# Performance work log

Hardware: AMD Instinct MI355X
Metric: run time of the kernel (lower is better)

## Reference

```python
import jax, jax.numpy as jnp
import numpy as np

D_MODEL = 1024
NHEAD = 16
HEAD_DIM = D_MODEL // NHEAD
ROPE_BASE = 10000.0


def setup_inputs() -> dict:
    key = jax.random.key(0)
    k1, k2, k3 = jax.random.split(key, 3)
    b, t = 2, 2048
    x = jax.random.normal(k1, (b, t, D_MODEL), dtype=jnp.float32)
    # weights stored as [in, out] so projection is x @ W (math-equivalent to torch Linear)
    w_qkv = jax.random.normal(k2, (D_MODEL, 3 * D_MODEL), dtype=jnp.float32) * (D_MODEL ** -0.5)
    w_out = jax.random.normal(k3, (D_MODEL, D_MODEL), dtype=jnp.float32) * (D_MODEL ** -0.5)
    return {"x": x, "w_qkv": w_qkv, "w_out": w_out}


def _rotate_half(x):
    # interleaved even/odd rotation, faithful to the torch code
    x1 = x[..., ::2]
    x2 = x[..., 1::2]
    return jnp.stack([-x2, x1], axis=-1).reshape(x.shape)


def _rope_cache(seq_len, dtype):
    half = HEAD_DIM // 2
    inv_freq = 1.0 / (ROPE_BASE ** (jnp.arange(half, dtype=jnp.float32) / float(half)))
    t = jnp.arange(seq_len, dtype=jnp.float32)
    freqs = jnp.einsum("i,j->ij", t, inv_freq)          # [T, half]
    emb = jnp.concatenate([freqs, freqs], axis=-1)        # [T, head_dim]
    return jnp.cos(emb).astype(dtype), jnp.sin(emb).astype(dtype)


def reference(x, w_qkv, w_out):
    b, t, c = x.shape
    qkv = x @ w_qkv                                       # [B, T, 3C]
    q, k, v = jnp.split(qkv, 3, axis=-1)
    def heads(z):
        return z.reshape(b, t, NHEAD, HEAD_DIM).transpose(0, 2, 1, 3)  # [B, H, T, Dh]
    q, k, v = heads(q), heads(k), heads(v)
    cos, sin = _rope_cache(t, q.dtype)                    # [T, Dh] broadcast over B, H
    q = q * cos + _rotate_half(q) * sin
    k = k * cos + _rotate_half(k) * sin
    scale = 1.0 / jnp.sqrt(jnp.asarray(HEAD_DIM, dtype=q.dtype))
    scores = jnp.einsum("bhqd,bhkd->bhqk", q, k) * scale  # [B, H, T, T]
    attn = jax.nn.softmax(scores, axis=-1)
    y = jnp.einsum("bhqk,bhkd->bhqd", attn, v)            # [B, H, T, Dh]
    y = y.transpose(0, 2, 1, 3).reshape(b, t, c)
    return y @ w_out
```

## Files before the change

### kernel.cpp

```cpp
#include <hip/hip_runtime.h>

typedef unsigned short u16;
typedef unsigned int u32;
typedef float f32x4 __attribute__((ext_vector_type(4)));
typedef float f32x16 __attribute__((ext_vector_type(16)));
typedef unsigned int u32x2 __attribute__((ext_vector_type(2)));
typedef __bf16 bf16x8 __attribute__((ext_vector_type(8)));

using gas_ptr = const __attribute__((address_space(1))) void*;
using las_ptr = __attribute__((address_space(3))) void*;

#define NH 16
#define HD 64
#define TSEQ 2048

__device__ __forceinline__ u16 f2bf(float f) {
  return __builtin_bit_cast(u16, (__bf16)f);
}
__device__ __forceinline__ u32 pk2bf(float a, float b) {
  return (u32)f2bf(a) | ((u32)f2bf(b) << 16);
}
__device__ __forceinline__ void pl_swap(u32& a, u32& b) {
  auto r = __builtin_amdgcn_permlane32_swap(a, b, false, false);
  u32x2 rv = __builtin_bit_cast(u32x2, r);
  a = rv[0];
  b = rv[1];
}

template <int NI>
__device__ __forceinline__ void stage_rows(const u16* __restrict__ src, size_t rstride,
                                           int row0, int col0, u16* lbuf, int tid) {
#pragma unroll
  for (int i = 0; i < NI; ++i) {
    int p = i * 256 + tid;
    int r = p >> 3, cst = p & 7;
    int csrc = cst ^ (r & 7);
    const u16* g = src + (size_t)(row0 + r) * rstride + col0 + csrc * 8;
    char* l = (char*)lbuf + (size_t)(i * 256 + (tid & ~63)) * 16;
    __builtin_amdgcn_global_load_lds((gas_ptr)g, (las_ptr)l, 16, 0, 0);
  }
}

__global__ void k_f32_to_bf16(const float* __restrict__ in, u16* __restrict__ out, int n4) {
  int i = blockIdx.x * blockDim.x + threadIdx.x;
  if (i >= n4) return;
  float4 v = ((const float4*)in)[i];
  ((uint2*)out)[i] = make_uint2(pk2bf(v.x, v.y), pk2bf(v.z, v.w));
}

__global__ void k_rope_tab(float2* __restrict__ tab) {
  int i = blockIdx.x * 256 + threadIdx.x;
  int t = i >> 5, j = i & 31;
  float inv = exp2f(-(float)j * 0.41524101186092028f);
  float s, c;
  sincosf((float)t * inv, &s, &c);
  tab[i] = make_float2(c, s);
}

__global__ void k_transpose_bf16(const float* __restrict__ in, u16* __restrict__ out,
                                 int R, int C) {
  __shared__ u16 lds[64 * 68];
  const int t = threadIdx.x;
  const int c0 = blockIdx.x * 64, r0 = blockIdx.y * 64;
  const int fc = (t & 15) * 4;
#pragma unroll
  for (int p = 0; p < 4; ++p) {
    int r = p * 16 + (t >> 4);
    float4 v = *(const float4*)&in[(size_t)(r0 + r) * C + c0 + fc];
    *(uint2*)&lds[r * 68 + fc] = make_uint2(pk2bf(v.x, v.y), pk2bf(v.z, v.w));
  }
  __syncthreads();
#pragma unroll
  for (int p = 0; p < 16; ++p) {
    int c = p * 4 + (t >> 6);
    int r = t & 63;
    out[(size_t)(c0 + c) * R + r0 + r] = lds[r * 68 + c];
  }
}

template <int MODE>
__global__ __launch_bounds__(256, 2) void k_gemm(const u16* __restrict__ A,
                                                 const u16* __restrict__ B,
                                                 float* __restrict__ outF,
                                                 u16* __restrict__ qb, u16* __restrict__ kb,
                                                 u16* __restrict__ vb,
                                                 const float2* __restrict__ rt, int N) {
  __shared__ __align__(16) u16 SH[32768];
  u16* Alb = SH;
  u16* Blb = SH + 16384;
  const int tid = threadIdx.x;
  const int lane = tid & 63;
  const int wv = tid >> 6, wr = wv >> 1, wc = wv & 1;
  const int m0 = blockIdx.y * 128, n0 = blockIdx.x * 128;

  f32x4 acc[4][4] = {};

  stage_rows<4>(A, 1024, m0, 0, Alb, tid);
  stage_rows<4>(B, 1024, n0, 0, Blb, tid);
  __syncthreads();

  for (int kt = 0; kt < 16; ++kt) {
    const int cur = kt & 1;
    if (kt < 15) {
      stage_rows<4>(A, 1024, m0, (kt + 1) * 64, Alb + (cur ^ 1) * 8192, tid);
      stage_rows<4>(B, 1024, n0, (kt + 1) * 64, Blb + (cur ^ 1) * 8192, tid);
    }
#pragma unroll
    for (int ks = 0; ks < 2; ++ks) {
      bf16x8 af[4], bfr[4];
#pragma unroll
      for (int mi = 0; mi < 4; ++mi) {
        int r = wr * 64 + mi * 16 + (lane & 15);
        int ch = (ks * 4 + (lane >> 4)) ^ (r & 7);
        af[mi] = *(const bf16x8*)((const char*)(Alb + cur * 8192) + r * 128 + ch * 16);
      }
#pragma unroll
      for (int ni = 0; ni < 4; ++ni) {
        int r = wc * 64 + ni * 16 + (lane & 15);
        int ch = (ks * 4 + (lane >> 4)) ^ (r & 7);
        bfr[ni] = *(const bf16x8*)((const char*)(Blb + cur * 8192) + r * 128 + ch * 16);
      }
#pragma unroll
      for (int mi = 0; mi < 4; ++mi)
#pragma unroll
        for (int ni = 0; ni < 4; ++ni)
          acc[mi][ni] =
              __builtin_amdgcn_mfma_f32_16x16x32_bf16(af[mi], bfr[ni], acc[mi][ni], 0, 0, 0);
    }
    __syncthreads();
  }

  if constexpr (MODE == 0) {
    const int which = n0 >> 10;
    u16* TB = SH;
    if (which < 2) {
      const float c0 = 0.18033688011112043f;
#pragma unroll
      for (int mi = 0; mi < 4; ++mi) {
        const int mb = wr * 64 + mi * 16 + ((lane >> 4) << 2);
#pragma unroll
        for (int ni = 0; ni < 4; ++ni) {
          const int nl = wc * 64 + ni * 16 + (lane & 15);
          const int d = (n0 + nl) & 63;
          const float sgn = (d & 1) ? 1.0f : -1.0f;
#pragma unroll
          for (int rr = 0; rr < 4; ++rr) {
            float v = acc[mi][ni][rr];
            float vp = __shfl_xor(v, 1);
            int tg = (m0 + mb + rr) & 2047;
            float2 cs = rt[tg * 32 + (d & 31)];
            float rv = v * cs.x + sgn * vp * cs.y;
            if (which == 0) rv *= c0;
            TB[(mb + rr) * 136 + nl] = f2bf(rv);
          }
        }
      }
      __syncthreads();
      const int m = tid >> 1, halfc = tid & 1;
      u16* dst = (which == 0 ? qb : kb) + (size_t)(m0 + m) * 1024 + (n0 & 1023) + halfc * 64;
      const u16* src = TB + m * 136 + halfc * 64;
#pragma unroll
      for (int j = 0; j < 8; ++j) *(uint4*)(dst + j * 8) = *(const uint4*)(src + j * 8);
    } else {
#pragma unroll
      for (int mi = 0; mi < 4; ++mi) {
        const int mb = wr * 64 + mi * 16 + ((lane >> 4) << 2);
#pragma unroll
        for (int ni = 0; ni < 4; ++ni) {
          const int nl = wc * 64 + ni * 16 + (lane & 15);
          uint2 w = make_uint2(pk2bf(acc[mi][ni][0], acc[mi][ni][1]),
                               pk2bf(acc[mi][ni][2], acc[mi][ni][3]));
          *(uint2*)(TB + nl * 136 + mb) = w;
        }
      }
      __syncthreads();
      const int nrow = tid >> 1, halfc = tid & 1;
      const int d = nrow & 63;
      const int hI = ((n0 - 2048) >> 6) + (nrow >> 6);
      const int bI = m0 >> 11;
      const int tb0 = (m0 & 2047) + halfc * 64;
      u16* dst = vb + ((size_t)((bI * NH + hI) * HD + d)) * TSEQ + tb0;
      const u16* src = TB + nrow * 136 + halfc * 64;
#pragma unroll
      for (int j = 0; j < 8; ++j) *(uint4*)(dst + j * 8) = *(const uint4*)(src + j * 8);
    }
  } else {
#pragma unroll
    for (int mi = 0; mi < 4; ++mi) {
      const int m = m0 + wr * 64 + mi * 16 + ((lane >> 4) << 2);
#pragma unroll
      for (int ni = 0; ni < 4; ++ni) {
        const int n = n0 + wc * 64 + ni * 16 + (lane & 15);
#pragma unroll
        for (int rr = 0; rr < 4; ++rr) outF[(size_t)(m + rr) * N + n] = acc[mi][ni][rr];
      }
    }
  }
}

__global__ __launch_bounds__(256, 2) void k_attn(const u16* __restrict__ qbuf,
                                                 const u16* __restrict__ kbuf,
                                                 const u16* __restrict__ vbuf,
                                                 u16* __restrict__ ybuf) {
  __shared__ __align__(16) u16 Kl[2][64 * 64];
  __shared__ __align__(16) u16 Vl[2][64 * 64];
  const int tid = threadIdx.x, lane = tid & 63, wv = tid >> 6;
  const int di = blockIdx.x;
  const int bh = (di & 7) * 4 + ((di >> 3) & 3);
  const int qt = di >> 5;
  const int b = bh >> 4, h = bh & 15;
  const int l31 = lane & 31, hi = lane >> 5;

  const u16* qrow = qbuf + (size_t)(b * TSEQ + qt * 128 + wv * 32 + l31) * 1024 + h * HD;
  const u16* kbase = kbuf + (size_t)b * TSEQ * 1024 + h * HD;
  const u16* vbase = vbuf + (size_t)bh * HD * TSEQ;

  bf16x8 qf[4];
#pragma unroll
  for (int s = 0; s < 4; ++s) qf[s] = *(const bf16x8*)(qrow + s * 16 + hi * 8);

  f32x16 o[2] = {};
  float psum = 0.f;

  stage_rows<2>(kbase, 1024, 0, 0, Kl[0], tid);
  stage_rows<2>(vbase, TSEQ, 0, 0, Vl[0], tid);
  __syncthreads();

  for (int it = 0; it < 32; ++it) {
    const int cur = it & 1;
    if (it < 31) {
      stage_rows<2>(kbase, 1024, (it + 1) * 64, 0, Kl[cur ^ 1], tid);
      stage_rows<2>(vbase, TSEQ, 0, (it + 1) * 64, Vl[cur ^ 1], tid);
    }
    bf16x8 pa[4];
#pragma unroll
    for (int kvt = 0; kvt < 2; ++kvt) {
      f32x16 sa = {};
#pragma unroll
      for (int s = 0; s < 4; ++s) {
        int r = kvt * 32 + l31;
        int ch = (s * 2 + hi) ^ (r & 7);
        bf16x8 kf = *(const bf16x8*)((const char*)Kl[cur] + r * 128 + ch * 16);
        sa = __builtin_amdgcn_mfma_f32_32x32x16_bf16(kf, qf[s], sa, 0, 0, 0);
      }
      float p[16];
#pragma unroll
      for (int r = 0; r < 16; ++r) {
        p[r] = exp2f(sa[r]);
        psum += p[r];
      }
#pragma unroll
      for (int s2 = 0; s2 < 2; ++s2) {
        const int pb = s2 * 8;
        u32 x = pk2bf(p[pb + 0], p[pb + 1]);
        u32 x2 = pk2bf(p[pb + 2], p[pb + 3]);
        u32 y = pk2bf(p[pb + 4], p[pb + 5]);
        u32 y2 = pk2bf(p[pb + 6], p[pb + 7]);
        pl_swap(x, y);
        pl_swap(x2, y2);
        bf16x8 frag;
        u32* fw = (u32*)&frag;
        fw[0] = x;
        fw[1] = x2;
        fw[2] = y;
        fw[3] = y2;
        pa[kvt * 2 + s2] = frag;
      }
    }
#pragma unroll
    for (int dt = 0; dt < 2; ++dt)
#pragma unroll
      for (int s = 0; s < 4; ++s) {
        int r = dt * 32 + l31;
        int ch = (s * 2 + hi) ^ (r & 7);
        bf16x8 vf = *(const bf16x8*)((const char*)Vl[cur] + r * 128 + ch * 16);
        o[dt] = __builtin_amdgcn_mfma_f32_32x32x16_bf16(pa[s], vf, o[dt], 0, 0, 0);
      }
    __syncthreads();
  }
  psum += __shfl_xor(psum, 32);
  float pinv = 1.0f / psum;
#pragma unroll
  for (int reg = 0; reg < 16; ++reg) {
    const int q = (reg & 3) + 8 * (reg >> 2) + 4 * hi;
    const float inv = __shfl(pinv, q);
    const int tq = qt * 128 + wv * 32 + q;
    const size_t rowb = ((size_t)b * TSEQ + tq) * 1024 + h * HD + l31;
    ybuf[rowb] = f2bf(o[0][reg] * inv);
    ybuf[rowb + 32] = f2bf(o[1][reg] * inv);
  }
}

extern "C" void kernel_launch(void* const* d_in, const int* in_sizes, int n_in, void* d_out,
                              int out_size, void* d_ws, size_t ws_size, hipStream_t stream) {
  const float* x = (const float*)d_in[0];
  const float* wqkv = (const float*)d_in[1];
  const float* wout = (const float*)d_in[2];
  float* out = (float*)d_out;
  char* ws = (char*)d_ws;

  u16* xb = (u16*)(ws);
  u16* wqkvT = (u16*)(ws + (8ull << 20));
  u16* woutT = (u16*)(ws + (14ull << 20));
  u16* qb = (u16*)(ws + (16ull << 20));
  u16* kb = (u16*)(ws + (24ull << 20));
  u16* vb = (u16*)(ws + (32ull << 20));
  u16* yb = (u16*)(ws + (40ull << 20));
  float2* rt = (float2*)(ws + (40ull << 20));

  k_f32_to_bf16<<<4096, 256, 0, stream>>>(x, xb, 1048576);
  k_rope_tab<<<256, 256, 0, stream>>>(rt);
  k_transpose_bf16<<<dim3(48, 16), 256, 0, stream>>>(wqkv, wqkvT, 1024, 3072);
  k_transpose_bf16<<<dim3(16, 16), 256, 0, stream>>>(wout, woutT, 1024, 1024);
  k_gemm<0><<<dim3(24, 32), 256, 0, stream>>>(xb, wqkvT, nullptr, qb, kb, vb, rt, 3072);
  k_attn<<<512, 256, 0, stream>>>(qb, kb, vb, yb);
  k_gemm<1><<<dim3(8, 32), 256, 0, stream>>>(yb, woutT, out, nullptr, nullptr, nullptr, nullptr,
                                             1024);
}
```

Measured before the change: 203.4 us.

## Halve attention block size, compute softmax denominator via MFMA, add setprio

The attention kernel now uses 128-thread blocks that each handle 64 query rows, launched as 1024 blocks instead of 512, with K/V staging adjusted to the smaller thread count. The softmax row sum moves from per-lane scalar adds plus cross-lane shuffles to an extra MFMA of the P tile against a ones vector, so the denominator comes out in the same register layout as the output. s_setprio hints are wrapped around the MFMA sections to favour matrix issue across waves. The aim is better load balance and VALU relief across CUs. In exchange, each block reuses its staged K/V tiles for half as many queries, which doubles global-to-LDS traffic, and it adds four MFMAs per iteration.

New measurement: 234.8 us. 15.4% more time.

```diff
diff --git a/kernel.cpp b/kernel.cpp
--- a/kernel.cpp
+++ b/kernel.cpp
@@ -27,16 +27,16 @@
   b = rv[1];
 }
 
-template <int NI>
+template <int NI, int THREADS = 256>
 __device__ __forceinline__ void stage_rows(const u16* __restrict__ src, size_t rstride,
                                            int row0, int col0, u16* lbuf, int tid) {
 #pragma unroll
   for (int i = 0; i < NI; ++i) {
-    int p = i * 256 + tid;
+    int p = i * THREADS + tid;
     int r = p >> 3, cst = p & 7;
     int csrc = cst ^ (r & 7);
     const u16* g = src + (size_t)(row0 + r) * rstride + col0 + csrc * 8;
-    char* l = (char*)lbuf + (size_t)(i * 256 + (tid & ~63)) * 16;
+    char* l = (char*)lbuf + (size_t)(i * THREADS + (tid & ~63)) * 16;
     __builtin_amdgcn_global_load_lds((gas_ptr)g, (las_ptr)l, 16, 0, 0);
   }
 }
@@ -198,7 +198,7 @@
   }
 }
 
-__global__ __launch_bounds__(256, 2) void k_attn(const u16* __restrict__ qbuf,
+__global__ __launch_bounds__(128, 2) void k_attn(const u16* __restrict__ qbuf,
                                                  const u16* __restrict__ kbuf,
                                                  const u16* __restrict__ vbuf,
                                                  u16* __restrict__ ybuf) {
@@ -211,7 +211,7 @@
   const int b = bh >> 4, h = bh & 15;
   const int l31 = lane & 31, hi = lane >> 5;
 
-  const u16* qrow = qbuf + (size_t)(b * TSEQ + qt * 128 + wv * 32 + l31) * 1024 + h * HD;
+  const u16* qrow = qbuf + (size_t)(b * TSEQ + qt * 64 + wv * 32 + l31) * 1024 + h * HD;
   const u16* kbase = kbuf + (size_t)b * TSEQ * 1024 + h * HD;
   const u16* vbase = vbuf + (size_t)bh * HD * TSEQ;
 
@@ -219,23 +219,31 @@
 #pragma unroll
   for (int s = 0; s < 4; ++s) qf[s] = *(const bf16x8*)(qrow + s * 16 + hi * 8);
 
+  bf16x8 vones;
+  {
+    u32 o1 = 0x3F803F80u;
+    u32* w = (u32*)&vones;
+    w[0] = o1; w[1] = o1; w[2] = o1; w[3] = o1;
+  }
+
   f32x16 o[2] = {};
-  float psum = 0.f;
-
-  stage_rows<2>(kbase, 1024, 0, 0, Kl[0], tid);
-  stage_rows<2>(vbase, TSEQ, 0, 0, Vl[0], tid);
+  f32x16 den = {};
+
+  stage_rows<4, 128>(kbase, 1024, 0, 0, Kl[0], tid);
+  stage_rows<4, 128>(vbase, TSEQ, 0, 0, Vl[0], tid);
   __syncthreads();
 
   for (int it = 0; it < 32; ++it) {
     const int cur = it & 1;
     if (it < 31) {
-      stage_rows<2>(kbase, 1024, (it + 1) * 64, 0, Kl[cur ^ 1], tid);
-      stage_rows<2>(vbase, TSEQ, 0, (it + 1) * 64, Vl[cur ^ 1], tid);
+      stage_rows<4, 128>(kbase, 1024, (it + 1) * 64, 0, Kl[cur ^ 1], tid);
+      stage_rows<4, 128>(vbase, TSEQ, 0, (it + 1) * 64, Vl[cur ^ 1], tid);
     }
     bf16x8 pa[4];
 #pragma unroll
     for (int kvt = 0; kvt < 2; ++kvt) {
       f32x16 sa = {};
+      __builtin_amdgcn_s_setprio(1);
 #pragma unroll
       for (int s = 0; s < 4; ++s) {
         int r = kvt * 32 + l31;
@@ -243,12 +251,10 @@
         bf16x8 kf = *(const bf16x8*)((const char*)Kl[cur] + r * 128 + ch * 16);
         sa = __builtin_amdgcn_mfma_f32_32x32x16_bf16(kf, qf[s], sa, 0, 0, 0);
       }
+      __builtin_amdgcn_s_setprio(0);
       float p[16];
 #pragma unroll
-      for (int r = 0; r < 16; ++r) {
-        p[r] = exp2f(sa[r]);
-        psum += p[r];
-      }
+      for (int r = 0; r < 16; ++r) p[r] = exp2f(sa[r]);
 #pragma unroll
       for (int s2 = 0; s2 < 2; ++s2) {
         const int pb = s2 * 8;
@@ -267,6 +273,7 @@
         pa[kvt * 2 + s2] = frag;
       }
     }
+    __builtin_amdgcn_s_setprio(1);
 #pragma unroll
     for (int dt = 0; dt < 2; ++dt)
 #pragma unroll
@@ -276,15 +283,17 @@
         bf16x8 vf = *(const bf16x8*)((const char*)Vl[cur] + r * 128 + ch * 16);
         o[dt] = __builtin_amdgcn_mfma_f32_32x32x16_bf16(pa[s], vf, o[dt], 0, 0, 0);
       }
+#pragma unroll
+    for (int s = 0; s < 4; ++s)
+      den = __builtin_amdgcn_mfma_f32_32x32x16_bf16(pa[s], vones, den, 0, 0, 0);
+    __builtin_amdgcn_s_setprio(0);
     __syncthreads();
   }
-  psum += __shfl_xor(psum, 32);
-  float pinv = 1.0f / psum;
 #pragma unroll
   for (int reg = 0; reg < 16; ++reg) {
     const int q = (reg & 3) + 8 * (reg >> 2) + 4 * hi;
-    const float inv = __shfl(pinv, q);
-    const int tq = qt * 128 + wv * 32 + q;
+    const float inv = 1.0f / den[reg];
+    const int tq = qt * 64 + wv * 32 + q;
     const size_t rowb = ((size_t)b * TSEQ + tq) * 1024 + h * HD + l31;
     ybuf[rowb] = f2bf(o[0][reg] * inv);
     ybuf[rowb + 32] = f2bf(o[1][reg] * inv);
@@ -313,7 +322,7 @@
   k_transpose_bf16<<<dim3(48, 16), 256, 0, stream>>>(wqkv, wqkvT, 1024, 3072);
   k_transpose_bf16<<<dim3(16, 16), 256, 0, stream>>>(wout, woutT, 1024, 1024);
   k_gemm<0><<<dim3(24, 32), 256, 0, stream>>>(xb, wqkvT, nullptr, qb, kb, vb, rt, 3072);
-  k_attn<<<512, 256, 0, stream>>>(qb, kb, vb, yb);
+  k_attn<<<1024, 128, 0, stream>>>(qb, kb, vb, yb);
   k_gemm<1><<<dim3(8, 32), 256, 0, stream>>>(yb, woutT, out, nullptr, nullptr, nullptr, nullptr,
                                              1024);
 }
```

## Split attention KV range across two wave groups per block with LDS reduction

Applied to the files above, without the earlier changes.

The attention kernel now launches 512 threads per block. Two groups of four waves each process half of the key/value sequence for the same 128 queries, each with its own double-buffered LDS tiles. The partial outputs and row sums are then combined through shared memory before normalization and the store. This doubles the waves available to hide latency on the grid of 512 blocks, at the cost of more LDS per block, an extra reduction and barrier, and possibly lower blocks per CU.

Result: faster. 199.3 us (-2.0%).

```diff
diff --git a/kernel.cpp b/kernel.cpp
--- a/kernel.cpp
+++ b/kernel.cpp
@@ -27,16 +27,16 @@
   b = rv[1];
 }
 
-template <int NI>
+template <int NI, int THREADS = 256>
 __device__ __forceinline__ void stage_rows(const u16* __restrict__ src, size_t rstride,
                                            int row0, int col0, u16* lbuf, int tid) {
 #pragma unroll
   for (int i = 0; i < NI; ++i) {
-    int p = i * 256 + tid;
+    int p = i * THREADS + tid;
     int r = p >> 3, cst = p & 7;
     int csrc = cst ^ (r & 7);
     const u16* g = src + (size_t)(row0 + r) * rstride + col0 + csrc * 8;
-    char* l = (char*)lbuf + (size_t)(i * 256 + (tid & ~63)) * 16;
+    char* l = (char*)lbuf + (size_t)(i * THREADS + (tid & ~63)) * 16;
     __builtin_amdgcn_global_load_lds((gas_ptr)g, (las_ptr)l, 16, 0, 0);
   }
 }
@@ -198,20 +198,25 @@
   }
 }
 
-__global__ __launch_bounds__(256, 2) void k_attn(const u16* __restrict__ qbuf,
+__global__ __launch_bounds__(512, 4) void k_attn(const u16* __restrict__ qbuf,
                                                  const u16* __restrict__ kbuf,
                                                  const u16* __restrict__ vbuf,
                                                  u16* __restrict__ ybuf) {
-  __shared__ __align__(16) u16 Kl[2][64 * 64];
-  __shared__ __align__(16) u16 Vl[2][64 * 64];
+  __shared__ __align__(16) u16 SH[32768];
   const int tid = threadIdx.x, lane = tid & 63, wv = tid >> 6;
+  const int half = wv >> 2, wvq = wv & 3;
+  const int t2 = tid & 255;
   const int di = blockIdx.x;
   const int bh = (di & 7) * 4 + ((di >> 3) & 3);
   const int qt = di >> 5;
   const int b = bh >> 4, h = bh & 15;
   const int l31 = lane & 31, hi = lane >> 5;
 
-  const u16* qrow = qbuf + (size_t)(b * TSEQ + qt * 128 + wv * 32 + l31) * 1024 + h * HD;
+  u16* const KLb = SH + half * 16384;
+  u16* const VLb = SH + half * 16384 + 8192;
+  const int r0 = half * 1024;
+
+  const u16* qrow = qbuf + (size_t)(b * TSEQ + qt * 128 + wvq * 32 + l31) * 1024 + h * HD;
   const u16* kbase = kbuf + (size_t)b * TSEQ * 1024 + h * HD;
   const u16* vbase = vbuf + (size_t)bh * HD * TSEQ;
 
@@ -222,15 +227,15 @@
   f32x16 o[2] = {};
   float psum = 0.f;
 
-  stage_rows<2>(kbase, 1024, 0, 0, Kl[0], tid);
-  stage_rows<2>(vbase, TSEQ, 0, 0, Vl[0], tid);
+  stage_rows<2, 256>(kbase, 1024, r0, 0, KLb, t2);
+  stage_rows<2, 256>(vbase, TSEQ, 0, r0, VLb, t2);
   __syncthreads();
 
-  for (int it = 0; it < 32; ++it) {
+  for (int it = 0; it < 16; ++it) {
     const int cur = it & 1;
-    if (it < 31) {
-      stage_rows<2>(kbase, 1024, (it + 1) * 64, 0, Kl[cur ^ 1], tid);
-      stage_rows<2>(vbase, TSEQ, 0, (it + 1) * 64, Vl[cur ^ 1], tid);
+    if (it < 15) {
+      stage_rows<2, 256>(kbase, 1024, r0 + (it + 1) * 64, 0, KLb + (cur ^ 1) * 4096, t2);
+      stage_rows<2, 256>(vbase, TSEQ, 0, r0 + (it + 1) * 64, VLb + (cur ^ 1) * 4096, t2);
     }
     bf16x8 pa[4];
 #pragma unroll
@@ -240,7 +245,7 @@
       for (int s = 0; s < 4; ++s) {
         int r = kvt * 32 + l31;
         int ch = (s * 2 + hi) ^ (r & 7);
-        bf16x8 kf = *(const bf16x8*)((const char*)Kl[cur] + r * 128 + ch * 16);
+        bf16x8 kf = *(const bf16x8*)((const char*)(KLb + cur * 4096) + r * 128 + ch * 16);
         sa = __builtin_amdgcn_mfma_f32_32x32x16_bf16(kf, qf[s], sa, 0, 0, 0);
       }
       float p[16];
@@ -273,21 +278,40 @@
       for (int s = 0; s < 4; ++s) {
         int r = dt * 32 + l31;
         int ch = (s * 2 + hi) ^ (r & 7);
-        bf16x8 vf = *(const bf16x8*)((const char*)Vl[cur] + r * 128 + ch * 16);
+        bf16x8 vf = *(const bf16x8*)((const char*)(VLb + cur * 4096) + r * 128 + ch * 16);
         o[dt] = __builtin_amdgcn_mfma_f32_32x32x16_bf16(pa[s], vf, o[dt], 0, 0, 0);
       }
     __syncthreads();
   }
-  psum += __shfl_xor(psum, 32);
-  float pinv = 1.0f / psum;
-#pragma unroll
-  for (int reg = 0; reg < 16; ++reg) {
-    const int q = (reg & 3) + 8 * (reg >> 2) + 4 * hi;
-    const float inv = __shfl(pinv, q);
-    const int tq = qt * 128 + wv * 32 + q;
-    const size_t rowb = ((size_t)b * TSEQ + tq) * 1024 + h * HD + l31;
-    ybuf[rowb] = f2bf(o[0][reg] * inv);
-    ybuf[rowb + 32] = f2bf(o[1][reg] * inv);
+
+  float* sc = (float*)SH;
+  if (half == 1) {
+    float* rec = sc + (wvq * 64 + lane) * 33;
+#pragma unroll
+    for (int dt = 0; dt < 2; ++dt)
+#pragma unroll
+      for (int reg = 0; reg < 16; ++reg) rec[dt * 16 + reg] = o[dt][reg];
+    rec[32] = psum;
+  }
+  __syncthreads();
+  if (half == 0) {
+    const float* rec = sc + (wvq * 64 + lane) * 33;
+#pragma unroll
+    for (int dt = 0; dt < 2; ++dt)
+#pragma unroll
+      for (int reg = 0; reg < 16; ++reg) o[dt][reg] += rec[dt * 16 + reg];
+    psum += rec[32];
+    psum += __shfl_xor(psum, 32);
+    float pinv = 1.0f / psum;
+#pragma unroll
+    for (int reg = 0; reg < 16; ++reg) {
+      const int q = (reg & 3) + 8 * (reg >> 2) + 4 * hi;
+      const float inv = __shfl(pinv, q);
+      const int tq = qt * 128 + wvq * 32 + q;
+      const size_t rowb = ((size_t)b * TSEQ + tq) * 1024 + h * HD + l31;
+      ybuf[rowb] = f2bf(o[0][reg] * inv);
+      ybuf[rowb + 32] = f2bf(o[1][reg] * inv);
+    }
   }
 }
 
@@ -313,7 +337,7 @@
   k_transpose_bf16<<<dim3(48, 16), 256, 0, stream>>>(wqkv, wqkvT, 1024, 3072);
   k_transpose_bf16<<<dim3(16, 16), 256, 0, stream>>>(wout, woutT, 1024, 1024);
   k_gemm<0><<<dim3(24, 32), 256, 0, stream>>>(xb, wqkvT, nullptr, qb, kb, vb, rt, 3072);
-  k_attn<<<512, 256, 0, stream>>>(qb, kb, vb, yb);
+  k_attn<<<512, 512, 0, stream>>>(qb, kb, vb, yb);
   k_gemm<1><<<dim3(8, 32), 256, 0, stream>>>(yb, woutT, out, nullptr, nullptr, nullptr, nullptr,
                                              1024);
 }
```
